# Kernel optimization log

Hardware: AMD Instinct MI355X
Metric: run time of the kernel (lower is better)

Reference implementation:

```python
import jax, jax.numpy as jnp
import numpy as np

D = 128          # lattice edge (Z = Y = X = 128)
S = 8            # state_size
H = 16           # hidden_size
IN = 7 * S       # own state + 6 neighbor states = 56


def setup_inputs() -> dict:
    key = jax.random.key(0)
    k0, k1, k2 = jax.random.split(key, 3)
    N = D * D * D
    states = jax.random.normal(k0, (N, S), dtype=jnp.float32)
    W1 = jax.random.normal(k1, (IN, H), dtype=jnp.float32) * (1.0 / np.sqrt(IN))
    b1 = jnp.zeros((H,), dtype=jnp.float32)
    W2 = jax.random.normal(k2, (H, S), dtype=jnp.float32) * (1.0 / np.sqrt(H))
    b2 = jnp.zeros((S,), dtype=jnp.float32)
    return {"states": states, "W1": W1, "b1": b1, "W2": W2, "b2": b2}


def reference(states, W1, b1, W2, b2):
    # linear index = z*(X*Y) + y*X + x  ->  grid layout (Z, Y, X, S)
    g = states.reshape(D, D, D, S)
    # 6-neighbor gather with periodic boundary (NEIGHBOR_DIRECTIONS order:
    # (-1,0,0),(1,0,0),(0,-1,0),(0,1,0),(0,0,-1),(0,0,1)); x->axis2, y->axis1, z->axis0.
    # roll(+1) along an axis fetches the neighbor in the -1 direction.
    nbrs = [
        jnp.roll(g,  1, axis=2),  # x-1
        jnp.roll(g, -1, axis=2),  # x+1
        jnp.roll(g,  1, axis=1),  # y-1
        jnp.roll(g, -1, axis=1),  # y+1
        jnp.roll(g,  1, axis=0),  # z-1
        jnp.roll(g, -1, axis=0),  # z+1
    ]
    inp = jnp.concatenate([g] + nbrs, axis=-1)          # (Z, Y, X, 56)
    h = jnp.tanh(jnp.einsum('zyxi,ih->zyxh', inp, W1) + b1)
    out = jnp.einsum('zyxh,hs->zyxs', h, W2) + b2        # (Z, Y, X, 8)
    return out.reshape(-1, S)
```

## Files before the change

### kernel.cpp

```cpp
#include <hip/hip_runtime.h>

#define DIM 128

typedef __attribute__((ext_vector_type(8))) short bf16x8;
typedef __attribute__((ext_vector_type(4))) float f32x4;
typedef __attribute__((ext_vector_type(4))) unsigned int u32x4;

static __device__ __forceinline__ unsigned short f2bf_rne(float f) {
    union { float f; unsigned int i; } c; c.f = f;
    unsigned int u = c.i;
    return (unsigned short)((u + 0x7fffu + ((u >> 16) & 1u)) >> 16);
}
static __device__ __forceinline__ float bf2f(unsigned short u) {
    union { unsigned int i; float f; } c; c.i = ((unsigned int)u) << 16;
    return c.f;
}
static __device__ __forceinline__ unsigned int fbits(float f) {
    union { float f; unsigned int i; } c; c.f = f; return c.i;
}
static __device__ __forceinline__ unsigned int pack_bf16_rne(float lo, float hi) {
    unsigned int ul = fbits(lo), uh = fbits(hi);
    unsigned int tl = ul + 0x7fffu + ((ul >> 16) & 1u);
    unsigned int th = uh + 0x7fffu + ((uh >> 16) & 1u);
    return __builtin_amdgcn_perm(th, tl, 0x07060302u);
}

struct Frags {
    bf16x8 w1h0, w1l0, w1h1, w1l1, w2h, w2l;
    f32x4 b1v, b2v;
};

static __device__ __forceinline__ void build_frags(
    const float* W1, const float* b1, const float* W2, const float* b2,
    int col, int quad, Frags& F)
{
#pragma unroll
    for (int j = 0; j < 8; ++j) {
        int k0 = quad * 8 + j;
        float w = W1[k0 * 16 + col];
        unsigned short hi = f2bf_rne(w);
        F.w1h0[j] = (short)hi;
        F.w1l0[j] = (short)f2bf_rne(w - bf2f(hi));

        int k1 = 32 + quad * 8 + j;
        float wv = (k1 < 56) ? W1[k1 * 16 + col] : 0.0f;
        hi = f2bf_rne(wv);
        F.w1h1[j] = (short)hi;
        F.w1l1[j] = (short)f2bf_rne(wv - bf2f(hi));

        float w2 = (j < 4 && col < 8) ? W2[(quad * 4 + j) * 8 + col] : 0.0f;
        hi = f2bf_rne(w2);
        F.w2h[j] = (short)hi;
        F.w2l[j] = (short)f2bf_rne(w2 - bf2f(hi));
    }
#pragma unroll
    for (int r = 0; r < 4; ++r) {
        F.b1v[r] = b1[quad * 4 + r];
        F.b2v[r] = (quad < 2) ? b2[quad * 4 + r] : 0.0f;
    }
}

__global__ __launch_bounds__(64) void setup_kernel(
    const float* __restrict__ W1, const float* __restrict__ b1,
    const float* __restrict__ W2, const float* __restrict__ b2,
    u32x4* __restrict__ ws)
{
    const int lane = threadIdx.x;
    Frags F;
    build_frags(W1, b1, W2, b2, lane & 15, lane >> 4, F);
    union { bf16x8 v; u32x4 u; } c;
    c.v = F.w1h0; ws[0 * 64 + lane] = c.u;
    c.v = F.w1l0; ws[1 * 64 + lane] = c.u;
    c.v = F.w1h1; ws[2 * 64 + lane] = c.u;
    c.v = F.w1l1; ws[3 * 64 + lane] = c.u;
    c.v = F.w2h;  ws[4 * 64 + lane] = c.u;
    c.v = F.w2l;  ws[5 * 64 + lane] = c.u;
    union { f32x4 v; u32x4 u; } b;
    b.v = F.b1v; ws[6 * 64 + lane] = b.u;
    b.v = F.b2v; ws[7 * 64 + lane] = b.u;
}

#define SLOT_STRIDE 2064
template<bool USE_WS>
__global__ __launch_bounds__(256, 4) void lattice_kernel(
    const float* __restrict__ states,
    const float* __restrict__ W1, const float* __restrict__ b1,
    const float* __restrict__ W2, const float* __restrict__ b2,
    float* __restrict__ out, const u32x4* __restrict__ ws)
{
    __shared__ __align__(16) unsigned char lds[15 * SLOT_STRIDE];

    const int tid  = threadIdx.x;
    const int lane = tid & 63;
    const int wave = tid >> 6;
    const int col  = lane & 15;
    const int quad = lane >> 4;

    Frags F;
    if (USE_WS) {
        union { u32x4 u; bf16x8 v; } c;
        c.u = ws[0 * 64 + lane]; F.w1h0 = c.v;
        c.u = ws[1 * 64 + lane]; F.w1l0 = c.v;
        c.u = ws[2 * 64 + lane]; F.w1h1 = c.v;
        c.u = ws[3 * 64 + lane]; F.w1l1 = c.v;
        c.u = ws[4 * 64 + lane]; F.w2h  = c.v;
        c.u = ws[5 * 64 + lane]; F.w2l  = c.v;
        union { u32x4 u; f32x4 v; } b;
        b.u = ws[6 * 64 + lane]; F.b1v = b.v;
        b.u = ws[7 * 64 + lane]; F.b2v = b.v;
    } else {
        build_frags(W1, b1, W2, b2, col, quad, F);
    }

    const int bI   = blockIdx.x;
    const int slab = bI & 7;
    const int inr  = bI >> 3;
    const int z    = slab * 16 + (inr >> 5);
    const int y0   = (inr & 31) << 2;

    f32x4 ga[7], gb[7];
    int   laddr[7];
#pragma unroll
    for (int i = 0; i < 7; ++i) {
        const int tk   = wave * 7 + i;
        const int slot = (tk < 20) ? (tk >> 1) : 11 + ((tk - 20) >> 1);
        const int half = tk & 1;
        int yr, zr;
        if (slot < 6)       { yr = (y0 - 1 + slot) & 127; zr = z; }
        else if (slot < 10) { yr = y0 + (slot - 6);       zr = (z - 1) & 127; }
        else                { yr = y0 + (slot - 11);      zr = (z + 1) & 127; }
        const int c = half * 64 + lane;
        const float* g = states + ((size_t)(zr * 16384 + yr * 128 + c) << 3);
        ga[i] = *(const f32x4*)g;
        gb[i] = *(const f32x4*)(g + 4);
        laddr[i] = slot * SLOT_STRIDE + c * 16;
    }
#pragma unroll
    for (int i = 0; i < 7; ++i) {
        u32x4 p;
        p[0] = __builtin_amdgcn_perm(fbits(ga[i][1]), fbits(ga[i][0]), 0x07060302u);
        p[1] = __builtin_amdgcn_perm(fbits(ga[i][3]), fbits(ga[i][2]), 0x07060302u);
        p[2] = __builtin_amdgcn_perm(fbits(gb[i][1]), fbits(gb[i][0]), 0x07060302u);
        p[3] = __builtin_amdgcn_perm(fbits(gb[i][3]), fbits(gb[i][2]), 0x07060302u);
        *(u32x4*)(lds + laddr[i]) = p;
    }
    __syncthreads();

    const int dxA   = (quad == 1) ? -1 : (quad == 2) ? 1 : 0;
    const int slotA = (quad == 3) ? wave : wave + 1;
    const int slotB = (quad == 1) ? 6 + wave : (quad == 2) ? 11 + wave : wave + 2;
    const int baseA = slotA * SLOT_STRIDE;
    const int baseB = slotB * SLOT_STRIDE;

    const int outrow = z * 16384 + (y0 + wave) * 128;

#pragma unroll
    for (int i = 0; i < 8; ++i) {
        const int X  = i << 4;
        const int xA = (X + col + dxA) & 127;
        bf16x8 s0f = *(const bf16x8*)(lds + baseA + xA * 16);
        bf16x8 s1f = *(const bf16x8*)(lds + baseB + (X + col) * 16);

        f32x4 acc = F.b1v;
        acc = __builtin_amdgcn_mfma_f32_16x16x32_bf16(F.w1h0, s0f, acc, 0, 0, 0);
        acc = __builtin_amdgcn_mfma_f32_16x16x32_bf16(F.w1l0, s0f, acc, 0, 0, 0);
        acc = __builtin_amdgcn_mfma_f32_16x16x32_bf16(F.w1h1, s1f, acc, 0, 0, 0);
        acc = __builtin_amdgcn_mfma_f32_16x16x32_bf16(F.w1l1, s1f, acc, 0, 0, 0);

        float h0t, h1t, h2t, h3t;
        {
            float e;
            e = __expf(2.0f * acc[0]); h0t = 1.0f - 2.0f * __builtin_amdgcn_rcpf(e + 1.0f);
            e = __expf(2.0f * acc[1]); h1t = 1.0f - 2.0f * __builtin_amdgcn_rcpf(e + 1.0f);
            e = __expf(2.0f * acc[2]); h2t = 1.0f - 2.0f * __builtin_amdgcn_rcpf(e + 1.0f);
            e = __expf(2.0f * acc[3]); h3t = 1.0f - 2.0f * __builtin_amdgcn_rcpf(e + 1.0f);
        }
        union { bf16x8 v; unsigned int u[4]; } hf;
        hf.u[0] = pack_bf16_rne(h0t, h1t);
        hf.u[1] = pack_bf16_rne(h2t, h3t);
        hf.u[2] = 0u;
        hf.u[3] = 0u;

        f32x4 acc2 = F.b2v;
        acc2 = __builtin_amdgcn_mfma_f32_16x16x32_bf16(F.w2h, hf.v, acc2, 0, 0, 0);
        acc2 = __builtin_amdgcn_mfma_f32_16x16x32_bf16(F.w2l, hf.v, acc2, 0, 0, 0);

        if (quad < 2) {
            f32x4* p = (f32x4*)(out + (size_t)(outrow + X + col) * 8 + quad * 4);
            __builtin_nontemporal_store(acc2, p);
        }
    }
}

extern "C" void kernel_launch(void* const* d_in, const int* in_sizes, int n_in,
                              void* d_out, int out_size, void* d_ws, size_t ws_size,
                              hipStream_t stream) {
    const float* states = (const float*)d_in[0];
    const float* W1     = (const float*)d_in[1];
    const float* b1     = (const float*)d_in[2];
    const float* W2     = (const float*)d_in[3];
    const float* b2     = (const float*)d_in[4];
    float* out          = (float*)d_out;

    const bool use_ws = ws_size >= (size_t)(8 * 64 * 16);
    if (use_ws) {
        hipLaunchKernelGGL(setup_kernel, dim3(1), dim3(64), 0, stream,
                           W1, b1, W2, b2, (u32x4*)d_ws);
        hipLaunchKernelGGL((lattice_kernel<true>), dim3(4096), dim3(256), 0, stream,
                           states, W1, b1, W2, b2, out, (const u32x4*)d_ws);
    } else {
        hipLaunchKernelGGL((lattice_kernel<false>), dim3(4096), dim3(256), 0, stream,
                           states, W1, b1, W2, b2, out, (const u32x4*)d_ws);
    }
}
```

Measured before the change: 135.3 us.

## Drop split-bf16 weight residuals and add halo-padded LDS rows

Removes the hi/lo bf16 splitting of W1 and W2, cutting the MFMA count per tile from six to three and halving the weight fragment registers and workspace size. The LDS rows get one-element halo padding on each side so the periodic x-wrap is served by extra stores instead of per-iteration modulo indexing. Pointer arithmetic is precomputed, and the occupancy hint rises from 4 to 5 blocks. The cost is lower precision in the weights, which may push results outside tolerance.

```diff
diff --git a/kernel.cpp b/kernel.cpp
--- a/kernel.cpp
+++ b/kernel.cpp
@@ -1,6 +1,7 @@
 #include <hip/hip_runtime.h>
 
 #define DIM 128
+#define SLOT_STRIDE 2096
 
 typedef __attribute__((ext_vector_type(8))) short bf16x8;
 typedef __attribute__((ext_vector_type(4))) float f32x4;
@@ -10,10 +11,6 @@
     union { float f; unsigned int i; } c; c.f = f;
     unsigned int u = c.i;
     return (unsigned short)((u + 0x7fffu + ((u >> 16) & 1u)) >> 16);
-}
-static __device__ __forceinline__ float bf2f(unsigned short u) {
-    union { unsigned int i; float f; } c; c.i = ((unsigned int)u) << 16;
-    return c.f;
 }
 static __device__ __forceinline__ unsigned int fbits(float f) {
     union { float f; unsigned int i; } c; c.f = f; return c.i;
@@ -26,7 +23,7 @@
 }
 
 struct Frags {
-    bf16x8 w1h0, w1l0, w1h1, w1l1, w2h, w2l;
+    bf16x8 w1h0, w1h1, w2h;
     f32x4 b1v, b2v;
 };
 
@@ -37,21 +34,11 @@
 #pragma unroll
     for (int j = 0; j < 8; ++j) {
         int k0 = quad * 8 + j;
-        float w = W1[k0 * 16 + col];
-        unsigned short hi = f2bf_rne(w);
-        F.w1h0[j] = (short)hi;
-        F.w1l0[j] = (short)f2bf_rne(w - bf2f(hi));
-
+        F.w1h0[j] = (short)f2bf_rne(W1[k0 * 16 + col]);
         int k1 = 32 + quad * 8 + j;
-        float wv = (k1 < 56) ? W1[k1 * 16 + col] : 0.0f;
-        hi = f2bf_rne(wv);
-        F.w1h1[j] = (short)hi;
-        F.w1l1[j] = (short)f2bf_rne(wv - bf2f(hi));
-
+        F.w1h1[j] = (short)f2bf_rne((k1 < 56) ? W1[k1 * 16 + col] : 0.0f);
         float w2 = (j < 4 && col < 8) ? W2[(quad * 4 + j) * 8 + col] : 0.0f;
-        hi = f2bf_rne(w2);
-        F.w2h[j] = (short)hi;
-        F.w2l[j] = (short)f2bf_rne(w2 - bf2f(hi));
+        F.w2h[j] = (short)f2bf_rne(w2);
     }
 #pragma unroll
     for (int r = 0; r < 4; ++r) {
@@ -70,19 +57,15 @@
     build_frags(W1, b1, W2, b2, lane & 15, lane >> 4, F);
     union { bf16x8 v; u32x4 u; } c;
     c.v = F.w1h0; ws[0 * 64 + lane] = c.u;
-    c.v = F.w1l0; ws[1 * 64 + lane] = c.u;
-    c.v = F.w1h1; ws[2 * 64 + lane] = c.u;
-    c.v = F.w1l1; ws[3 * 64 + lane] = c.u;
-    c.v = F.w2h;  ws[4 * 64 + lane] = c.u;
-    c.v = F.w2l;  ws[5 * 64 + lane] = c.u;
+    c.v = F.w1h1; ws[1 * 64 + lane] = c.u;
+    c.v = F.w2h;  ws[2 * 64 + lane] = c.u;
     union { f32x4 v; u32x4 u; } b;
-    b.v = F.b1v; ws[6 * 64 + lane] = b.u;
-    b.v = F.b2v; ws[7 * 64 + lane] = b.u;
+    b.v = F.b1v; ws[3 * 64 + lane] = b.u;
+    b.v = F.b2v; ws[4 * 64 + lane] = b.u;
 }
 
-#define SLOT_STRIDE 2064
 template<bool USE_WS>
-__global__ __launch_bounds__(256, 4) void lattice_kernel(
+__global__ __launch_bounds__(256, 5) void lattice_kernel(
     const float* __restrict__ states,
     const float* __restrict__ W1, const float* __restrict__ b1,
     const float* __restrict__ W2, const float* __restrict__ b2,
@@ -92,7 +75,7 @@
 
     const int tid  = threadIdx.x;
     const int lane = tid & 63;
-    const int wave = tid >> 6;
+    const int w    = __builtin_amdgcn_readfirstlane(tid >> 6);
     const int col  = lane & 15;
     const int quad = lane >> 4;
 
@@ -100,14 +83,11 @@
     if (USE_WS) {
         union { u32x4 u; bf16x8 v; } c;
         c.u = ws[0 * 64 + lane]; F.w1h0 = c.v;
-        c.u = ws[1 * 64 + lane]; F.w1l0 = c.v;
-        c.u = ws[2 * 64 + lane]; F.w1h1 = c.v;
-        c.u = ws[3 * 64 + lane]; F.w1l1 = c.v;
-        c.u = ws[4 * 64 + lane]; F.w2h  = c.v;
-        c.u = ws[5 * 64 + lane]; F.w2l  = c.v;
+        c.u = ws[1 * 64 + lane]; F.w1h1 = c.v;
+        c.u = ws[2 * 64 + lane]; F.w2h  = c.v;
         union { u32x4 u; f32x4 v; } b;
-        b.u = ws[6 * 64 + lane]; F.b1v = b.v;
-        b.u = ws[7 * 64 + lane]; F.b2v = b.v;
+        b.u = ws[3 * 64 + lane]; F.b1v = b.v;
+        b.u = ws[4 * 64 + lane]; F.b2v = b.v;
     } else {
         build_frags(W1, b1, W2, b2, col, quad, F);
     }
@@ -119,53 +99,52 @@
     const int y0   = (inr & 31) << 2;
 
     f32x4 ga[7], gb[7];
-    int   laddr[7];
 #pragma unroll
     for (int i = 0; i < 7; ++i) {
-        const int tk   = wave * 7 + i;
+        const int tk   = w * 7 + i;
         const int slot = (tk < 20) ? (tk >> 1) : 11 + ((tk - 20) >> 1);
         const int half = tk & 1;
         int yr, zr;
         if (slot < 6)       { yr = (y0 - 1 + slot) & 127; zr = z; }
         else if (slot < 10) { yr = y0 + (slot - 6);       zr = (z - 1) & 127; }
         else                { yr = y0 + (slot - 11);      zr = (z + 1) & 127; }
-        const int c = half * 64 + lane;
-        const float* g = states + ((size_t)(zr * 16384 + yr * 128 + c) << 3);
-        ga[i] = *(const f32x4*)g;
-        gb[i] = *(const f32x4*)(g + 4);
-        laddr[i] = slot * SLOT_STRIDE + c * 16;
+        const float* g = states + ((size_t)(zr * 16384 + yr * 128 + half * 64) << 3);
+        ga[i] = *(const f32x4*)(g + (lane << 3));
+        gb[i] = *(const f32x4*)(g + (lane << 3) + 4);
     }
 #pragma unroll
     for (int i = 0; i < 7; ++i) {
+        const int tk   = w * 7 + i;
+        const int slot = (tk < 20) ? (tk >> 1) : 11 + ((tk - 20) >> 1);
+        const int half = tk & 1;
         u32x4 p;
         p[0] = __builtin_amdgcn_perm(fbits(ga[i][1]), fbits(ga[i][0]), 0x07060302u);
         p[1] = __builtin_amdgcn_perm(fbits(ga[i][3]), fbits(ga[i][2]), 0x07060302u);
         p[2] = __builtin_amdgcn_perm(fbits(gb[i][1]), fbits(gb[i][0]), 0x07060302u);
         p[3] = __builtin_amdgcn_perm(fbits(gb[i][3]), fbits(gb[i][2]), 0x07060302u);
-        *(u32x4*)(lds + laddr[i]) = p;
+        const int base = slot * SLOT_STRIDE;
+        *(u32x4*)(lds + base + ((half * 64 + lane + 1) << 4)) = p;
+        if (half == 0 && lane == 0)  *(u32x4*)(lds + base + 2064) = p;
+        if (half == 1 && lane == 63) *(u32x4*)(lds + base) = p;
     }
     __syncthreads();
 
     const int dxA   = (quad == 1) ? -1 : (quad == 2) ? 1 : 0;
-    const int slotA = (quad == 3) ? wave : wave + 1;
-    const int slotB = (quad == 1) ? 6 + wave : (quad == 2) ? 11 + wave : wave + 2;
-    const int baseA = slotA * SLOT_STRIDE;
-    const int baseB = slotB * SLOT_STRIDE;
+    const int slotA = (quad == 3) ? w : w + 1;
+    const int slotB = (quad == 1) ? 6 + w : (quad == 2) ? 11 + w : w + 2;
+    const unsigned char* pA = lds + slotA * SLOT_STRIDE + ((col + dxA + 1) << 4);
+    const unsigned char* pB = lds + slotB * SLOT_STRIDE + ((col + 1) << 4);
 
-    const int outrow = z * 16384 + (y0 + wave) * 128;
+    float* pO = out + (size_t)((z * 16384 + (y0 + w) * 128 + col) * 8 + quad * 4);
 
 #pragma unroll
     for (int i = 0; i < 8; ++i) {
-        const int X  = i << 4;
-        const int xA = (X + col + dxA) & 127;
-        bf16x8 s0f = *(const bf16x8*)(lds + baseA + xA * 16);
-        bf16x8 s1f = *(const bf16x8*)(lds + baseB + (X + col) * 16);
+        bf16x8 s0f = *(const bf16x8*)(pA + (i << 8));
+        bf16x8 s1f = *(const bf16x8*)(pB + (i << 8));
 
         f32x4 acc = F.b1v;
         acc = __builtin_amdgcn_mfma_f32_16x16x32_bf16(F.w1h0, s0f, acc, 0, 0, 0);
-        acc = __builtin_amdgcn_mfma_f32_16x16x32_bf16(F.w1l0, s0f, acc, 0, 0, 0);
         acc = __builtin_amdgcn_mfma_f32_16x16x32_bf16(F.w1h1, s1f, acc, 0, 0, 0);
-        acc = __builtin_amdgcn_mfma_f32_16x16x32_bf16(F.w1l1, s1f, acc, 0, 0, 0);
 
         float h0t, h1t, h2t, h3t;
         {
@@ -183,11 +162,9 @@
 
         f32x4 acc2 = F.b2v;
         acc2 = __builtin_amdgcn_mfma_f32_16x16x32_bf16(F.w2h, hf.v, acc2, 0, 0, 0);
-        acc2 = __builtin_amdgcn_mfma_f32_16x16x32_bf16(F.w2l, hf.v, acc2, 0, 0, 0);
 
         if (quad < 2) {
-            f32x4* p = (f32x4*)(out + (size_t)(outrow + X + col) * 8 + quad * 4);
-            __builtin_nontemporal_store(acc2, p);
+            __builtin_nontemporal_store(acc2, (f32x4*)(pO + (i << 7)));
         }
     }
 }
@@ -202,7 +179,7 @@
     const float* b2     = (const float*)d_in[4];
     float* out          = (float*)d_out;
 
-    const bool use_ws = ws_size >= (size_t)(8 * 64 * 16);
+    const bool use_ws = ws_size >= (size_t)(5 * 64 * 16);
     if (use_ws) {
         hipLaunchKernelGGL(setup_kernel, dim3(1), dim3(64), 0, stream,
                            W1, b1, W2, b2, (u32x4*)d_ws);
```

After: 117.9 us. -12.8%, faster.
